# Kernel tuning notes

Hardware: AMD Instinct MI355X
Metric: run time of the kernel (lower is better)

## Reference

```python
import jax, jax.numpy as jnp
import numpy as np

NUM_MASHUP = 50000
NUM_API = 50000
NUM_DOMAIN = 500
MC = 768   # mashup_embed_channels
AC = 768   # api_embed_channels
DC = 768   # domain_embed_channels
FEAT = 128 # feature_dim
BETA = 0.5
NLAYERS = 3
E = 1600000  # bipartite invocations (one direction)
BATCH = 1024


def setup_inputs() -> dict:
    key = jax.random.key(0)
    ks = jax.random.split(key, 16)
    s = 0.02
    return {
        "x": jax.random.normal(ks[0], (BATCH, MC), dtype=jnp.float32),
        "mashup_embed": jax.random.normal(ks[1], (NUM_MASHUP, MC), dtype=jnp.float32),
        "domain_embed": jax.random.normal(ks[2], (NUM_DOMAIN, DC), dtype=jnp.float32),
        "api_embed": jax.random.normal(ks[3], (NUM_API, AC), dtype=jnp.float32),
        "W_sde": jax.random.normal(ks[4], (MC, FEAT), dtype=jnp.float32) * s,
        "b_sde": jnp.zeros((FEAT,), jnp.float32),
        "W_val": jax.random.normal(ks[5], (DC, FEAT), dtype=jnp.float32) * s,
        "b_val": jnp.zeros((FEAT,), jnp.float32),
        "W_key": jax.random.normal(ks[6], (DC, FEAT), dtype=jnp.float32) * s,
        "b_key": jnp.zeros((FEAT,), jnp.float32),
        "W_sie": jax.random.normal(ks[7], (AC, FEAT), dtype=jnp.float32) * s,
        "b_sie": jnp.zeros((FEAT,), jnp.float32),
        "edge_src": jax.random.randint(ks[8], (E,), 0, NUM_MASHUP, dtype=jnp.int32),
        "edge_dst": jax.random.randint(ks[9], (E,), 0, NUM_API, dtype=jnp.int32),
    }


def _sig_lin(h, W, b):
    # nn.Linear + Sigmoid
    return jax.nn.sigmoid(h @ W + b)


def _lightgcn(emb, row, col, num_nodes, num_layers):
    # PyG LightGCN.get_embedding: mean of layer-0..L embeddings with
    # symmetric gcn_norm propagation over the bipartite graph.
    ones = jnp.ones(row.shape, emb.dtype)
    deg = jax.ops.segment_sum(ones, row, num_segments=num_nodes)
    dinv = jnp.where(deg > 0, jax.lax.rsqrt(deg), 0.0)
    norm = dinv[row] * dinv[col]  # [2E]
    alpha = 1.0 / (num_layers + 1)
    x_l = emb
    out = emb * alpha
    for _ in range(num_layers):
        # message x[row]*norm scattered to col (graph is symmetric)
        x_l = jax.ops.segment_sum(x_l[row] * norm[:, None], col, num_segments=num_nodes)
        out = out + x_l * alpha
    return out


def reference(x, mashup_embed, domain_embed, api_embed,
              W_sde, b_sde, W_val, b_val, W_key, b_key, W_sie, b_sie,
              edge_src, edge_dst):
    batch = x.shape[0]
    # --- attention pooling over domain embeddings (SDE branch) ---
    v_mi = _sig_lin(x, W_sde, b_sde)                 # [B, F]
    v_value = _sig_lin(domain_embed, W_val, b_val)   # [D, F]
    v_key = _sig_lin(domain_embed, W_key, b_key)     # [D, F]
    al = v_mi @ v_key.T                              # [B, D]
    alpha = al / jnp.sum(al, axis=1, keepdims=True)  # normalized (no softmax)
    s_m = alpha @ v_value                            # [B, F]
    z_m = (1.0 - BETA) * s_m + BETA * v_mi           # [B, F]
    # --- LightGCN propagation over mashup-api bipartite graph ---
    v_m = _sig_lin(mashup_embed, W_sde, b_sde)       # [Nm, F]
    v_s = _sig_lin(api_embed, W_sie, b_sie)          # [Na, F]
    emb = jnp.concatenate([v_m, v_s], axis=0)        # [N, F]
    num_nodes = NUM_MASHUP + NUM_API
    src = edge_src.astype(jnp.int32)
    dst = edge_dst.astype(jnp.int32) + NUM_MASHUP
    row = jnp.concatenate([src, dst])                # [2E] symmetric edges
    col = jnp.concatenate([dst, src])
    out = _lightgcn(emb, row, col, num_nodes, NLAYERS)
    O = out[NUM_MASHUP:]                             # [Na, F]
    # --- dot-product scoring ---
    pred = z_m @ O.T                                 # [B, Na]
    return pred
```

## Files before the change

### kernel.cpp

```cpp
#include <hip/hip_runtime.h>
#include <hip/hip_bf16.h>
#include <cstddef>
#include <cstdint>

#define NM 50000
#define NA 50000
#define ND 500
#define FEAT 128
#define KDIM 768
#define BATCH 1024
#define NEDGE 1600000
#define MD 128

#define NBIN 196
#define CAP 10240
#define F1B 400
#define F1E (NEDGE / F1B)

#define PB64 782

typedef __bf16 bf16_t;
typedef bf16_t bf16x8 __attribute__((ext_vector_type(8)));
typedef bf16_t bf16x4 __attribute__((ext_vector_type(4)));
typedef float f32x4 __attribute__((ext_vector_type(4)));
typedef float f32x2 __attribute__((ext_vector_type(2)));
typedef unsigned short u16;
typedef unsigned char u8;

__device__ __forceinline__ float sigf(float x) { return 1.0f / (1.0f + __expf(-x)); }

__device__ __forceinline__ float4 dec4fp8(uint32_t w) {
  f32x2 lo = __builtin_amdgcn_cvt_pk_f32_fp8(w, false);
  f32x2 hi = __builtin_amdgcn_cvt_pk_f32_fp8(w, true);
  return make_float4(lo[0], lo[1], hi[0], hi[1]);
}
__device__ __forceinline__ u8 enc1fp8(float a) {
  return (u8)(__builtin_amdgcn_cvt_pk_fp8_f32(a, a, 0, false) & 0xff);
}

__global__ __launch_bounds__(256) void fill_bin(
    const int* __restrict__ src, const int* __restrict__ dst,
    int* __restrict__ bcur, uint32_t* __restrict__ rec )
{
  __shared__ uint32_t edg[F1E];
  __shared__ int hist[2 * NBIN];
  __shared__ int base[2 * NBIN];
  const int tid = threadIdx.x;
  for (int i = tid; i < 2 * NBIN; i += 256) hist[i] = 0;
  __syncthreads();
  const int e0 = blockIdx.x * F1E;
  for (int i = tid; i < F1E; i += 256) {
    int s = __builtin_nontemporal_load(&src[e0 + i]);
    int d = __builtin_nontemporal_load(&dst[e0 + i]);
    edg[i] = ((uint32_t)s << 16) | (uint32_t)d;
    atomicAdd(&hist[s >> 8], 1);
    atomicAdd(&hist[NBIN + (d >> 8)], 1);
  }
  __syncthreads();
  for (int i = tid; i < 2 * NBIN; i += 256) {
    int c = hist[i];
    base[i] = c ? atomicAdd(&bcur[i], c) : 0;
    hist[i] = 0;
  }
  __syncthreads();
  for (int i = tid; i < F1E; i += 256) {
    uint32_t e = edg[i];
    int s = (int)(e >> 16), d = (int)(e & 0xffffu);
    int bm = s >> 8, ba = NBIN + (d >> 8);
    int rm = base[bm] + atomicAdd(&hist[bm], 1);
    int ra = base[ba] + atomicAdd(&hist[ba], 1);
    if (rm < CAP) rec[(size_t)bm * CAP + rm] = e;
    if (ra < CAP) rec[(size_t)ba * CAP + ra] = ((uint32_t)d << 16) | (uint32_t)s;
  }
}

__global__ __launch_bounds__(256) void fill_ell2(
    const uint32_t* __restrict__ rec, const int* __restrict__ bcur,
    u16* __restrict__ adjm, u16* __restrict__ adja,
    int* __restrict__ cnt_m, int* __restrict__ cnt_a)
{
  __shared__ int cnt256[256];
  const int g = blockIdx.x;
  const int side = g >= NBIN;
  const int bin = side ? g - NBIN : g;
  u16* adj = side ? adja : adjm;
  int* cnt = side ? cnt_a : cnt_m;
  cnt256[threadIdx.x] = 0;
  __syncthreads();
  int n = bcur[g]; if (n > CAP) n = CAP;
  const uint32_t* rb = rec + (size_t)g * CAP;
  for (int i = threadIdx.x; i < n; i += 256) {
    uint32_t r = rb[i];
    int node = (int)(r >> 16);
    int rk = atomicAdd(&cnt256[node & 255], 1);
    if (rk < MD) adj[(size_t)node * MD + rk] = (u16)(r & 0xffffu);
  }
  __syncthreads();
  int node = bin * 256 + threadIdx.x;
  if (node < NM) cnt[node] = cnt256[threadIdx.x];
}

__global__ __launch_bounds__(256) void util_kernel(
    const float* __restrict__ W0, const float* __restrict__ W1,
    const float* __restrict__ W2, const float* __restrict__ W3,
    bf16_t* __restrict__ T0, bf16_t* __restrict__ T1,
    bf16_t* __restrict__ T2, bf16_t* __restrict__ T3,
    const int* __restrict__ cnt_m, const int* __restrict__ cnt_a,
    float* __restrict__ dm, float* __restrict__ da)
{
  const int b = blockIdx.x;
  if (b < 512) {
    const float* W = (b < 128) ? W0 : (b < 256) ? W1 : (b < 384) ? W2 : W3;
    bf16_t* T      = (b < 128) ? T0 : (b < 256) ? T1 : (b < 384) ? T2 : T3;
    int c = b & 127;
    for (int k = threadIdx.x; k < KDIM; k += 256)
      T[(size_t)c * KDIM + k] = (bf16_t)W[(size_t)k * FEAT + c];
  } else {
    int i = (b - 512) * 256 + threadIdx.x;
    if (i < NM) { int c = cnt_m[i]; dm[i] = c > 0 ? rsqrtf((float)c) : 0.f; }
    if (i < NA) { int c = cnt_a[i]; da[i] = c > 0 ? rsqrtf((float)c) : 0.f; }
  }
}

template<int OM>
__device__ __forceinline__ void proj_body(
    const float* __restrict__ A, const bf16_t* __restrict__ Wt,
    const float* __restrict__ bias, void* __restrict__ Cout, int M, int rowBase,
    const float* __restrict__ rowscale, bf16_t* __restrict__ C2)
{
  __shared__ bf16x8 sm[768];
  const int tid = threadIdx.x;
  const int lane = tid & 63;
  const int wid = tid >> 6;

  f32x4 acc[2][4];
  #pragma unroll
  for (int m = 0; m < 2; ++m)
    #pragma unroll
    for (int n = 0; n < 4; ++n)
      acc[m][n] = (f32x4){0.f, 0.f, 0.f, 0.f};

  const int arow = ((tid >> 6) << 4) + (tid & 15);
  const int k8 = (tid >> 4) & 3;
  int arg = rowBase + arow; if (arg > M - 1) arg = M - 1;
  const float*  aptr  = A  + (size_t)arg * KDIM + k8 * 8;
  const bf16_t* bptr0 = Wt + (size_t)arow * KDIM + k8 * 8;
  const bf16_t* bptr1 = Wt + (size_t)(arow + 64) * KDIM + k8 * 8;

  float4 pa0 = *(const float4*)aptr;
  float4 pa1 = *(const float4*)(aptr + 4);
  bf16x8 pb0 = *(const bf16x8*)bptr0;
  bf16x8 pb1 = *(const bf16x8*)bptr1;

  const int fm0 = (wid >> 1) * 2, fn0 = (wid & 1) * 4;

  for (int kt = 0; kt < KDIM / 32; ++kt) {
    bf16x8 w;
    w[0] = (bf16_t)pa0.x; w[1] = (bf16_t)pa0.y; w[2] = (bf16_t)pa0.z; w[3] = (bf16_t)pa0.w;
    w[4] = (bf16_t)pa1.x; w[5] = (bf16_t)pa1.y; w[6] = (bf16_t)pa1.z; w[7] = (bf16_t)pa1.w;
    sm[tid] = w;
    sm[256 + tid] = pb0;
    sm[512 + tid] = pb1;
    __syncthreads();
    if (kt + 1 < KDIM / 32) {
      const int ko = (kt + 1) * 32;
      pa0 = *(const float4*)(aptr + ko);
      pa1 = *(const float4*)(aptr + ko + 4);
      pb0 = *(const bf16x8*)(bptr0 + ko);
      pb1 = *(const bf16x8*)(bptr1 + ko);
    }
    bf16x8 a[2], b[4];
    #pragma unroll
    for (int m = 0; m < 2; ++m) a[m] = sm[(fm0 + m) * 64 + lane];
    #pragma unroll
    for (int n = 0; n < 4; ++n) b[n] = sm[256 + (fn0 + n) * 64 + lane];
    #pragma unroll
    for (int m = 0; m < 2; ++m)
      #pragma unroll
      for (int n = 0; n < 4; ++n)
        acc[m][n] = __builtin_amdgcn_mfma_f32_16x16x32_bf16(a[m], b[n], acc[m][n], 0, 0, 0);
    __syncthreads();
  }

  const int wRow = (wid >> 1) * 32, wCol = (wid & 1) * 64;
  const int r0 = (lane >> 4) * 4, cc = lane & 15;
  #pragma unroll
  for (int n = 0; n < 4; ++n) {
    int col = wCol + n * 16 + cc;
    float bb = bias[col];
    #pragma unroll
    for (int m = 0; m < 2; ++m) {
      #pragma unroll
      for (int r = 0; r < 4; ++r) {
        int row = rowBase + wRow + m * 16 + r0 + r;
        if (row < M) {
          float v = sigf(acc[m][n][r] + bb);
          float sc = rowscale ? rowscale[row] : 1.0f;
          if constexpr (OM == 2)
            ((u8*)Cout)[(size_t)row * FEAT + col] = enc1fp8(v * sc);
          else
            ((float*)Cout)[(size_t)row * FEAT + col] = v * sc;
          if (C2) C2[(size_t)row * FEAT + col] = (bf16_t)(0.25f * v);
        }
      }
    }
  }
}

__global__ __launch_bounds__(256) void proj_all(
    const float* __restrict__ mashup, const float* __restrict__ api,
    const float* __restrict__ x, const float* __restrict__ domain,
    const bf16_t* __restrict__ wt0, const bf16_t* __restrict__ wt1,
    const bf16_t* __restrict__ wt2, const bf16_t* __restrict__ wt3,
    const float* __restrict__ bsde, const float* __restrict__ bkey,
    const float* __restrict__ bval, const float* __restrict__ bsie,
    u8* __restrict__ M0y8, u8* __restrict__ y0a8,
    float* __restrict__ vmi, float* __restrict__ vkey, float* __restrict__ vval,
    const float* __restrict__ dm, const float* __restrict__ da,
    bf16_t* __restrict__ outA)
{
  const int b = blockIdx.x;
  if (b < PB64)
    proj_body<2>(mashup, wt0, bsde, M0y8, NM, b * 64, dm, nullptr);
  else if (b < 2 * PB64)
    proj_body<2>(api, wt3, bsie, y0a8, NA, (b - PB64) * 64, da, outA);
  else if (b < 2 * PB64 + 16)
    proj_body<0>(x, wt0, bsde, vmi, BATCH, (b - 2 * PB64) * 64, nullptr, nullptr);
  else if (b < 2 * PB64 + 24)
    proj_body<0>(domain, wt1, bkey, vkey, ND, (b - 2 * PB64 - 16) * 64, nullptr, nullptr);
  else
    proj_body<0>(domain, wt2, bval, vval, ND, (b - 2 * PB64 - 24) * 64, nullptr, nullptr);
}

__global__ __launch_bounds__(256) void attn_kernel(
    const float* __restrict__ vmi, const float* __restrict__ vkey,
    const float* __restrict__ vval, bf16_t* __restrict__ zm)
{
  const int i = blockIdx.x;
  const int tid = threadIdx.x;
  __shared__ float vs[FEAT];
  __shared__ float al[ND];
  __shared__ float red[4];
  __shared__ float ps[256];
  __shared__ float totS;
  if (tid < FEAT) vs[tid] = vmi[(size_t)i * FEAT + tid];
  __syncthreads();
  float part = 0.f;
  for (int j = tid; j < ND; j += 256) {
    const float* kr = vkey + (size_t)j * FEAT;
    float dot = 0.f;
    #pragma unroll 8
    for (int k = 0; k < FEAT; k += 4) {
      float4 kv = *(const float4*)(kr + k);
      dot += vs[k] * kv.x + vs[k + 1] * kv.y + vs[k + 2] * kv.z + vs[k + 3] * kv.w;
    }
    al[j] = dot;
    part += dot;
  }
  #pragma unroll
  for (int o = 32; o > 0; o >>= 1) part += __shfl_down(part, o, 64);
  if ((tid & 63) == 0) red[tid >> 6] = part;
  __syncthreads();
  if (tid == 0) totS = red[0] + red[1] + red[2] + red[3];
  const int f = tid & 127, h = tid >> 7;
  float s = 0.f;
  const float* vv = vval + (size_t)h * 250 * FEAT + f;
  #pragma unroll 5
  for (int j = 0; j < 250; ++j) s += al[h * 250 + j] * vv[(size_t)j * FEAT];
  ps[tid] = s;
  __syncthreads();
  if (tid < FEAT) {
    float z = 0.5f * ((ps[tid] + ps[128 + tid]) / totS + vs[tid]);
    zm[(size_t)i * FEAT + tid] = (bf16_t)z;
  }
}

__device__ __forceinline__ float4 gatherF8(const uint32_t* __restrict__ base32,
                                           const u16* __restrict__ row,
                                           int n, int half)
{
  float4 acc = make_float4(0.f, 0.f, 0.f, 0.f);
  int j = half;
  while (j + 14 < n) {
    int u[8];
    #pragma unroll
    for (int q = 0; q < 8; ++q) u[q] = row[j + 2 * q];
    uint32_t w[8];
    #pragma unroll
    for (int q = 0; q < 8; ++q) w[q] = base32[(size_t)u[q] * 32];
    #pragma unroll
    for (int q = 0; q < 8; ++q) {
      float4 v = dec4fp8(w[q]);
      acc.x += v.x; acc.y += v.y; acc.z += v.z; acc.w += v.w;
    }
    j += 16;
  }
  while (j < n) {
    float4 v = dec4fp8(base32[(size_t)row[j] * 32]);
    acc.x += v.x; acc.y += v.y; acc.z += v.z; acc.w += v.w;
    j += 2;
  }
  return acc;
}

#define REDUCE_HALVES(acc)                    \
  acc.x += __shfl_xor(acc.x, 32);             \
  acc.y += __shfl_xor(acc.y, 32);             \
  acc.z += __shfl_xor(acc.z, 32);             \
  acc.w += __shfl_xor(acc.w, 32);

__global__ __launch_bounds__(256) void prop_p1(
    const uint32_t* __restrict__ M0y8, const uint32_t* __restrict__ y0a8,
    uint32_t* __restrict__ y01a8,
    const u16* __restrict__ adja, const int* __restrict__ cnt_a,
    const float* __restrict__ da)
{
  const int a = blockIdx.x * 4 + (threadIdx.x >> 6);
  const int lane = threadIdx.x & 63;
  const int half = lane >> 5, sl = lane & 31;
  int n = cnt_a[a]; if (n > MD) n = MD;
  float4 acc = gatherF8(M0y8 + sl, adja + (size_t)a * MD, n, half);
  REDUCE_HALVES(acc)
  if (half == 0) {
    const float d = da[a];
    const float s2 = d * d;
    float4 b = dec4fp8(y0a8[(size_t)a * 32 + sl]);
    uint32_t o = __builtin_amdgcn_cvt_pk_fp8_f32(b.x + s2 * acc.x, b.y + s2 * acc.y, 0, false);
    o = __builtin_amdgcn_cvt_pk_fp8_f32(b.z + s2 * acc.z, b.w + s2 * acc.w, o, true);
    y01a8[(size_t)a * 32 + sl] = o;
  }
}

__global__ __launch_bounds__(256) void prop_p2(
    const uint32_t* __restrict__ y01a8, const uint32_t* __restrict__ M0y8,
    uint32_t* __restrict__ Sy8,
    const u16* __restrict__ adjm, const int* __restrict__ cnt_m,
    const float* __restrict__ dm)
{
  const int m = blockIdx.x * 4 + (threadIdx.x >> 6);
  const int lane = threadIdx.x & 63;
  const int half = lane >> 5, sl = lane & 31;
  int n = cnt_m[m]; if (n > MD) n = MD;
  float4 acc = gatherF8(y01a8 + sl, adjm + (size_t)m * MD, n, half);
  REDUCE_HALVES(acc)
  if (half == 0) {
    const float d = dm[m];
    const float s2 = d * d;
    float4 b = dec4fp8(M0y8[(size_t)m * 32 + sl]);
    uint32_t o = __builtin_amdgcn_cvt_pk_fp8_f32(b.x + s2 * acc.x, b.y + s2 * acc.y, 0, false);
    o = __builtin_amdgcn_cvt_pk_fp8_f32(b.z + s2 * acc.z, b.w + s2 * acc.w, o, true);
    Sy8[(size_t)m * 32 + sl] = o;
  }
}

__global__ __launch_bounds__(256) void prop_p3(
    const uint32_t* __restrict__ Sy8, const bf16_t* __restrict__ outA,
    bf16_t* __restrict__ Obf,
    const u16* __restrict__ adja, const int* __restrict__ cnt_a,
    const float* __restrict__ da)
{
  const int a = blockIdx.x * 4 + (threadIdx.x >> 6);
  const int lane = threadIdx.x & 63;
  const int half = lane >> 5, sl = lane & 31;
  int n = cnt_a[a]; if (n > MD) n = MD;
  float4 acc = gatherF8(Sy8 + sl, adja + (size_t)a * MD, n, half);
  REDUCE_HALVES(acc)
  if (half == 0) {
    const float q = 0.25f * da[a];
    bf16x4 pv = *(const bf16x4*)(outA + (size_t)a * FEAT + 4 * sl);
    bf16x4 o;
    o[0] = (bf16_t)((float)pv[0] + q * acc.x);
    o[1] = (bf16_t)((float)pv[1] + q * acc.y);
    o[2] = (bf16_t)((float)pv[2] + q * acc.z);
    o[3] = (bf16_t)((float)pv[3] + q * acc.w);
    *(bf16x4*)(Obf + (size_t)a * FEAT + 4 * sl) = o;
  }
}

__global__ __launch_bounds__(256) void pred_mfma(
    const bf16_t* __restrict__ Z, const bf16_t* __restrict__ O,
    float* __restrict__ out)
{
  const int lane = threadIdx.x & 63;
  const int wid = threadIdx.x >> 6;
  const int nBase = blockIdx.x * 256 + wid * 64;
  const int cc = lane & 15;
  const int kOff = (lane >> 4) * 8;

  bf16x8 b[4][4];
  #pragma unroll
  for (int n = 0; n < 4; ++n) {
    int c = nBase + n * 16 + cc;
    if (c > NA - 1) c = NA - 1;
    #pragma unroll
    for (int kk = 0; kk < 4; ++kk)
      b[n][kk] = *(const bf16x8*)(O + (size_t)c * FEAT + kk * 32 + kOff);
  }

  const int r0 = (lane >> 4) * 4;
  #pragma unroll
  for (int it = 0; it < 4; ++it) {
    const int iBase = blockIdx.y * 256 + it * 64;
    f32x4 acc[4][4];
    #pragma unroll
    for (int m = 0; m < 4; ++m)
      #pragma unroll
      for (int n = 0; n < 4; ++n)
        acc[m][n] = (f32x4){0.f, 0.f, 0.f, 0.f};

    #pragma unroll
    for (int kk = 0; kk < 4; ++kk) {
      bf16x8 a[4];
      #pragma unroll
      for (int m = 0; m < 4; ++m)
        a[m] = *(const bf16x8*)(Z + (size_t)(iBase + cc + m * 16) * FEAT + kk * 32 + kOff);
      #pragma unroll
      for (int m = 0; m < 4; ++m)
        #pragma unroll
        for (int n = 0; n < 4; ++n)
          acc[m][n] = __builtin_amdgcn_mfma_f32_16x16x32_bf16(a[m], b[n][kk], acc[m][n], 0, 0, 0);
    }

    #pragma unroll
    for (int n = 0; n < 4; ++n) {
      int col = nBase + n * 16 + cc;
      if (col < NA) {
        #pragma unroll
        for (int m = 0; m < 4; ++m) {
          #pragma unroll
          for (int r = 0; r < 4; ++r) {
            int row = iBase + m * 16 + r0 + r;
            __builtin_nontemporal_store(acc[m][n][r], &out[(size_t)row * NA + col]);
          }
        }
      }
    }
  }
}

static inline char* alignup(char* p, size_t a) {
  return (char*)(((uintptr_t)p + a - 1) & ~(uintptr_t)(a - 1));
}

extern "C" void kernel_launch(void* const* d_in, const int* in_sizes, int n_in,
                              void* d_out, int out_size, void* d_ws, size_t ws_size,
                              hipStream_t stream) {
  const float* x      = (const float*)d_in[0];
  const float* mashup = (const float*)d_in[1];
  const float* domain = (const float*)d_in[2];
  const float* api    = (const float*)d_in[3];
  const float* Wsde   = (const float*)d_in[4];
  const float* bsde   = (const float*)d_in[5];
  const float* Wval   = (const float*)d_in[6];
  const float* bval   = (const float*)d_in[7];
  const float* Wkey   = (const float*)d_in[8];
  const float* bkey   = (const float*)d_in[9];
  const float* Wsie   = (const float*)d_in[10];
  const float* bsie   = (const float*)d_in[11];
  const int* esrc     = (const int*)d_in[12];
  const int* edst     = (const int*)d_in[13];
  float* out = (float*)d_out;

  char* p = (char*)d_ws;
  u8*     M0y8  = (u8*)p; p += (size_t)NM * FEAT;
  u8*     y0a8  = (u8*)p; p += (size_t)NA * FEAT;
  u8*     y01a8 = (u8*)p; p += (size_t)NA * FEAT;
  u8*     Sy8   = (u8*)p; p += (size_t)NM * FEAT;
  bf16_t* outA  = (bf16_t*)p; p += (size_t)NA * FEAT * 2;
  bf16_t* Obf   = (bf16_t*)p; p += (size_t)NA * FEAT * 2;
  u16*    adjm  = (u16*)p;    p += (size_t)NM * MD * 2;
  u16*    adja  = (u16*)p;    p += (size_t)NA * MD * 2;
  float*  vmi   = (float*)p;  p += (size_t)BATCH * FEAT * 4;
  float*  vkey  = (float*)p;  p += (size_t)ND * FEAT * 4;
  float*  vval  = (float*)p;  p += (size_t)ND * FEAT * 4;
  bf16_t* zm    = (bf16_t*)p; p += (size_t)BATCH * FEAT * 2;
  int* cnt_m = (int*)p; p += (size_t)NM * 4;
  int* cnt_a = (int*)p; p += (size_t)NA * 4;
  float* dm  = (float*)p; p += (size_t)NM * 4;
  float* da  = (float*)p; p += (size_t)NA * 4;
  int* bcur  = (int*)p; p += 512 * 4;
  p = alignup(p, 16);
  bf16_t* wt0 = (bf16_t*)p; p += (size_t)FEAT * KDIM * 2;
  bf16_t* wt1 = (bf16_t*)p; p += (size_t)FEAT * KDIM * 2;
  bf16_t* wt2 = (bf16_t*)p; p += (size_t)FEAT * KDIM * 2;
  bf16_t* wt3 = (bf16_t*)p; p += (size_t)FEAT * KDIM * 2;
  uint32_t* rec = (uint32_t*)M0y8;

  hipMemsetAsync(bcur, 0, 512 * sizeof(int), stream);

  fill_bin<<<F1B, 256, 0, stream>>>(esrc, edst, bcur, rec);
  fill_ell2<<<2 * NBIN, 256, 0, stream>>>(rec, bcur, adjm, adja, cnt_m, cnt_a);
  util_kernel<<<512 + (NM + 255) / 256, 256, 0, stream>>>(
      Wsde, Wkey, Wval, Wsie, wt0, wt1, wt2, wt3, cnt_m, cnt_a, dm, da);

  proj_all<<<2 * PB64 + 32, 256, 0, stream>>>(
      mashup, api, x, domain, wt0, wt1, wt2, wt3,
      bsde, bkey, bval, bsie, M0y8, y0a8, vmi, vkey, vval, dm, da, outA);

  attn_kernel<<<BATCH, 256, 0, stream>>>(vmi, vkey, vval, zm);

  prop_p1<<<NA / 4, 256, 0, stream>>>((const uint32_t*)M0y8, (const uint32_t*)y0a8,
                                      (uint32_t*)y01a8, adja, cnt_a, da);
  prop_p2<<<NM / 4, 256, 0, stream>>>((const uint32_t*)y01a8, (const uint32_t*)M0y8,
                                      (uint32_t*)Sy8, adjm, cnt_m, dm);
  prop_p3<<<NA / 4, 256, 0, stream>>>((const uint32_t*)Sy8, outA, Obf,
                                      adja, cnt_a, da);

  pred_mfma<<<dim3((NA + 255) / 256, BATCH / 256), 256, 0, stream>>>(zm, Obf, out);
}
```

Before: 421.3 us.

## Rewrite projection GEMM as per-wave 16-row tiles without shared memory

The projection kernel no longer stages A and W tiles through LDS with block-wide barriers. Each wave now computes a 16x128 output tile on its own, loading A rows directly into registers and reading the transposed bf16 weights straight from global memory (L2/L1 cached) for all 8 column fragments. This removes the __syncthreads and LDS traffic. In exchange, each wave issues more global weight loads, since W is no longer shared across the 4 waves of a block, and it holds more accumulator registers.

```diff
diff --git a/kernel.cpp b/kernel.cpp
--- a/kernel.cpp
+++ b/kernel.cpp
@@ -123,85 +123,60 @@
 }
 
 template<int OM>
-__device__ __forceinline__ void proj_body(
+__device__ __forceinline__ void proj_wave(
     const float* __restrict__ A, const bf16_t* __restrict__ Wt,
     const float* __restrict__ bias, void* __restrict__ Cout, int M, int rowBase,
     const float* __restrict__ rowscale, bf16_t* __restrict__ C2)
 {
-  __shared__ bf16x8 sm[768];
-  const int tid = threadIdx.x;
-  const int lane = tid & 63;
-  const int wid = tid >> 6;
-
-  f32x4 acc[2][4];
+  const int lane = threadIdx.x & 63;
+  const int r = lane & 15;
+  const int kg = (lane >> 4) * 8;
+
+  int rowL = rowBase + r; if (rowL > M - 1) rowL = M - 1;
+  const float*  ap = A  + (size_t)rowL * KDIM + kg;
+  const bf16_t* bp = Wt + (size_t)r * KDIM + kg;
+
+  f32x4 acc[8];
   #pragma unroll
-  for (int m = 0; m < 2; ++m)
-    #pragma unroll
-    for (int n = 0; n < 4; ++n)
-      acc[m][n] = (f32x4){0.f, 0.f, 0.f, 0.f};
-
-  const int arow = ((tid >> 6) << 4) + (tid & 15);
-  const int k8 = (tid >> 4) & 3;
-  int arg = rowBase + arow; if (arg > M - 1) arg = M - 1;
-  const float*  aptr  = A  + (size_t)arg * KDIM + k8 * 8;
-  const bf16_t* bptr0 = Wt + (size_t)arow * KDIM + k8 * 8;
-  const bf16_t* bptr1 = Wt + (size_t)(arow + 64) * KDIM + k8 * 8;
-
-  float4 pa0 = *(const float4*)aptr;
-  float4 pa1 = *(const float4*)(aptr + 4);
-  bf16x8 pb0 = *(const bf16x8*)bptr0;
-  bf16x8 pb1 = *(const bf16x8*)bptr1;
-
-  const int fm0 = (wid >> 1) * 2, fn0 = (wid & 1) * 4;
+  for (int n = 0; n < 8; ++n) acc[n] = (f32x4){0.f, 0.f, 0.f, 0.f};
+
+  float4 pa0 = *(const float4*)ap;
+  float4 pa1 = *(const float4*)(ap + 4);
 
   for (int kt = 0; kt < KDIM / 32; ++kt) {
-    bf16x8 w;
-    w[0] = (bf16_t)pa0.x; w[1] = (bf16_t)pa0.y; w[2] = (bf16_t)pa0.z; w[3] = (bf16_t)pa0.w;
-    w[4] = (bf16_t)pa1.x; w[5] = (bf16_t)pa1.y; w[6] = (bf16_t)pa1.z; w[7] = (bf16_t)pa1.w;
-    sm[tid] = w;
-    sm[256 + tid] = pb0;
-    sm[512 + tid] = pb1;
-    __syncthreads();
+    const int k0 = kt * 32;
+    bf16x8 a;
+    a[0] = (bf16_t)pa0.x; a[1] = (bf16_t)pa0.y; a[2] = (bf16_t)pa0.z; a[3] = (bf16_t)pa0.w;
+    a[4] = (bf16_t)pa1.x; a[5] = (bf16_t)pa1.y; a[6] = (bf16_t)pa1.z; a[7] = (bf16_t)pa1.w;
     if (kt + 1 < KDIM / 32) {
-      const int ko = (kt + 1) * 32;
-      pa0 = *(const float4*)(aptr + ko);
-      pa1 = *(const float4*)(aptr + ko + 4);
-      pb0 = *(const bf16x8*)(bptr0 + ko);
-      pb1 = *(const bf16x8*)(bptr1 + ko);
-    }
-    bf16x8 a[2], b[4];
-    #pragma unroll
-    for (int m = 0; m < 2; ++m) a[m] = sm[(fm0 + m) * 64 + lane];
-    #pragma unroll
-    for (int n = 0; n < 4; ++n) b[n] = sm[256 + (fn0 + n) * 64 + lane];
-    #pragma unroll
-    for (int m = 0; m < 2; ++m)
-      #pragma unroll
-      for (int n = 0; n < 4; ++n)
-        acc[m][n] = __builtin_amdgcn_mfma_f32_16x16x32_bf16(a[m], b[n], acc[m][n], 0, 0, 0);
-    __syncthreads();
-  }
-
-  const int wRow = (wid >> 1) * 32, wCol = (wid & 1) * 64;
-  const int r0 = (lane >> 4) * 4, cc = lane & 15;
+      pa0 = *(const float4*)(ap + k0 + 32);
+      pa1 = *(const float4*)(ap + k0 + 36);
+    }
+    bf16x8 b[8];
+    #pragma unroll
+    for (int n = 0; n < 8; ++n)
+      b[n] = *(const bf16x8*)(bp + (size_t)n * 16 * KDIM + k0);
+    #pragma unroll
+    for (int n = 0; n < 8; ++n)
+      acc[n] = __builtin_amdgcn_mfma_f32_16x16x32_bf16(a, b[n], acc[n], 0, 0, 0);
+  }
+
+  const int r0 = (lane >> 4) * 4;
   #pragma unroll
-  for (int n = 0; n < 4; ++n) {
-    int col = wCol + n * 16 + cc;
+  for (int n = 0; n < 8; ++n) {
+    int col = n * 16 + r;
     float bb = bias[col];
     #pragma unroll
-    for (int m = 0; m < 2; ++m) {
-      #pragma unroll
-      for (int r = 0; r < 4; ++r) {
-        int row = rowBase + wRow + m * 16 + r0 + r;
-        if (row < M) {
-          float v = sigf(acc[m][n][r] + bb);
-          float sc = rowscale ? rowscale[row] : 1.0f;
-          if constexpr (OM == 2)
-            ((u8*)Cout)[(size_t)row * FEAT + col] = enc1fp8(v * sc);
-          else
-            ((float*)Cout)[(size_t)row * FEAT + col] = v * sc;
-          if (C2) C2[(size_t)row * FEAT + col] = (bf16_t)(0.25f * v);
-        }
+    for (int rr = 0; rr < 4; ++rr) {
+      int row = rowBase + r0 + rr;
+      if (row < M) {
+        float v = sigf(acc[n][rr] + bb);
+        float sc = rowscale ? rowscale[row] : 1.0f;
+        if constexpr (OM == 2)
+          ((u8*)Cout)[(size_t)row * FEAT + col] = enc1fp8(v * sc);
+        else
+          ((float*)Cout)[(size_t)row * FEAT + col] = v * sc;
+        if (C2) C2[(size_t)row * FEAT + col] = (bf16_t)(0.25f * v);
       }
     }
   }
@@ -220,16 +195,17 @@
     bf16_t* __restrict__ outA)
 {
   const int b = blockIdx.x;
+  const int w = threadIdx.x >> 6;
   if (b < PB64)
-    proj_body<2>(mashup, wt0, bsde, M0y8, NM, b * 64, dm, nullptr);
+    proj_wave<2>(mashup, wt0, bsde, M0y8, NM, b * 64 + w * 16, dm, nullptr);
   else if (b < 2 * PB64)
-    proj_body<2>(api, wt3, bsie, y0a8, NA, (b - PB64) * 64, da, outA);
+    proj_wave<2>(api, wt3, bsie, y0a8, NA, (b - PB64) * 64 + w * 16, da, outA);
   else if (b < 2 * PB64 + 16)
-    proj_body<0>(x, wt0, bsde, vmi, BATCH, (b - 2 * PB64) * 64, nullptr, nullptr);
+    proj_wave<0>(x, wt0, bsde, vmi, BATCH, (b - 2 * PB64) * 64 + w * 16, nullptr, nullptr);
   else if (b < 2 * PB64 + 24)
-    proj_body<0>(domain, wt1, bkey, vkey, ND, (b - 2 * PB64 - 16) * 64, nullptr, nullptr);
+    proj_wave<0>(domain, wt1, bkey, vkey, ND, (b - 2 * PB64 - 16) * 64 + w * 16, nullptr, nullptr);
   else
-    proj_body<0>(domain, wt2, bval, vval, ND, (b - 2 * PB64 - 24) * 64, nullptr, nullptr);
+    proj_wave<0>(domain, wt2, bval, vval, ND, (b - 2 * PB64 - 24) * 64 + w * 16, nullptr, nullptr);
 }
 
 __global__ __launch_bounds__(256) void attn_kernel(
```

Measured after the change: 534.2 us. 26.8% more time.

## Double-buffer projection GEMM tiles with direct global-to-LDS loads

Applied to the files above, without the earlier changes.

The projection GEMM now loads A (fp32) and W tiles straight into LDS with global_load_lds, double-buffered, and waits on vmcnt so the next tile's load overlaps the current tile's MFMAs. The fp32-to-bf16 conversion of A moves from the store side to the LDS read side. This removes the register staging round trip and one sync per iteration, but doubles LDS use and relies on hand-written waitcnt and barrier ordering being correct.

```diff
diff --git a/kernel.cpp b/kernel.cpp
--- a/kernel.cpp
+++ b/kernel.cpp
@@ -18,6 +18,7 @@
 #define F1E (NEDGE / F1B)
 
 #define PB64 782
+#define PKT  24
 
 typedef __bf16 bf16_t;
 typedef bf16_t bf16x8 __attribute__((ext_vector_type(8)));
@@ -36,6 +37,12 @@
 }
 __device__ __forceinline__ u8 enc1fp8(float a) {
   return (u8)(__builtin_amdgcn_cvt_pk_fp8_f32(a, a, 0, false) & 0xff);
+}
+
+__device__ __forceinline__ void gll16(const void* g, void* l) {
+  __builtin_amdgcn_global_load_lds(
+      (const __attribute__((address_space(1))) unsigned int*)g,
+      (__attribute__((address_space(3))) unsigned int*)l, 16, 0, 0);
 }
 
 __global__ __launch_bounds__(256) void fill_bin(
@@ -128,11 +135,16 @@
     const float* __restrict__ bias, void* __restrict__ Cout, int M, int rowBase,
     const float* __restrict__ rowscale, bf16_t* __restrict__ C2)
 {
-  __shared__ bf16x8 sm[768];
+  __shared__ alignas(16) char smraw[2][16384];
   const int tid = threadIdx.x;
   const int lane = tid & 63;
   const int wid = tid >> 6;
 
+  int arow = rowBase + wid * 16 + (lane & 15); if (arow > M - 1) arow = M - 1;
+  const float*  asrc  = A  + (size_t)arow * KDIM + ((lane >> 4) * 8);
+  const bf16_t* bsrc0 = Wt + (size_t)((2 * wid) * 16 + (lane & 15)) * KDIM + ((lane >> 4) * 8);
+  const bf16_t* bsrc1 = Wt + (size_t)((2 * wid + 1) * 16 + (lane & 15)) * KDIM + ((lane >> 4) * 8);
+
   f32x4 acc[2][4];
   #pragma unroll
   for (int m = 0; m < 2; ++m)
@@ -140,46 +152,56 @@
     for (int n = 0; n < 4; ++n)
       acc[m][n] = (f32x4){0.f, 0.f, 0.f, 0.f};
 
-  const int arow = ((tid >> 6) << 4) + (tid & 15);
-  const int k8 = (tid >> 4) & 3;
-  int arg = rowBase + arow; if (arg > M - 1) arg = M - 1;
-  const float*  aptr  = A  + (size_t)arg * KDIM + k8 * 8;
-  const bf16_t* bptr0 = Wt + (size_t)arow * KDIM + k8 * 8;
-  const bf16_t* bptr1 = Wt + (size_t)(arow + 64) * KDIM + k8 * 8;
-
-  float4 pa0 = *(const float4*)aptr;
-  float4 pa1 = *(const float4*)(aptr + 4);
-  bf16x8 pb0 = *(const bf16x8*)bptr0;
-  bf16x8 pb1 = *(const bf16x8*)bptr1;
-
-  const int fm0 = (wid >> 1) * 2, fn0 = (wid & 1) * 4;
-
-  for (int kt = 0; kt < KDIM / 32; ++kt) {
-    bf16x8 w;
-    w[0] = (bf16_t)pa0.x; w[1] = (bf16_t)pa0.y; w[2] = (bf16_t)pa0.z; w[3] = (bf16_t)pa0.w;
-    w[4] = (bf16_t)pa1.x; w[5] = (bf16_t)pa1.y; w[6] = (bf16_t)pa1.z; w[7] = (bf16_t)pa1.w;
-    sm[tid] = w;
-    sm[256 + tid] = pb0;
-    sm[512 + tid] = pb1;
-    __syncthreads();
-    if (kt + 1 < KDIM / 32) {
-      const int ko = (kt + 1) * 32;
-      pa0 = *(const float4*)(aptr + ko);
-      pa1 = *(const float4*)(aptr + ko + 4);
-      pb0 = *(const bf16x8*)(bptr0 + ko);
-      pb1 = *(const bf16x8*)(bptr1 + ko);
-    }
+  const int fA = (wid >> 1) * 2;
+  const int fB = (wid & 1) * 4;
+
+  int cur = 0;
+  {
+    char* base = smraw[0];
+    gll16(asrc,      base + wid * 2048);
+    gll16(asrc + 4,  base + wid * 2048 + 1024);
+    gll16(bsrc0,     base + 8192 + (2 * wid) * 1024);
+    gll16(bsrc1,     base + 8192 + (2 * wid + 1) * 1024);
+  }
+
+  for (int kt = 0; kt < PKT; ++kt) {
+    if (kt + 1 < PKT) {
+      const int k0 = (kt + 1) * 32;
+      char* base = smraw[cur ^ 1];
+      gll16(asrc + k0,      base + wid * 2048);
+      gll16(asrc + k0 + 4,  base + wid * 2048 + 1024);
+      gll16(bsrc0 + k0,     base + 8192 + (2 * wid) * 1024);
+      gll16(bsrc1 + k0,     base + 8192 + (2 * wid + 1) * 1024);
+      asm volatile("s_waitcnt vmcnt(4)" ::: "memory");
+    } else {
+      asm volatile("s_waitcnt vmcnt(0)" ::: "memory");
+    }
+    __builtin_amdgcn_s_barrier();
+    asm volatile("" ::: "memory");
+
+    const char* bb = smraw[cur];
     bf16x8 a[2], b[4];
     #pragma unroll
-    for (int m = 0; m < 2; ++m) a[m] = sm[(fm0 + m) * 64 + lane];
-    #pragma unroll
-    for (int n = 0; n < 4; ++n) b[n] = sm[256 + (fn0 + n) * 64 + lane];
+    for (int m = 0; m < 2; ++m) {
+      f32x4 lo = *(const f32x4*)(bb + (fA + m) * 2048 + lane * 16);
+      f32x4 hi = *(const f32x4*)(bb + (fA + m) * 2048 + 1024 + lane * 16);
+      bf16x8 t;
+      t[0] = (bf16_t)lo[0]; t[1] = (bf16_t)lo[1]; t[2] = (bf16_t)lo[2]; t[3] = (bf16_t)lo[3];
+      t[4] = (bf16_t)hi[0]; t[5] = (bf16_t)hi[1]; t[6] = (bf16_t)hi[2]; t[7] = (bf16_t)hi[3];
+      a[m] = t;
+    }
+    #pragma unroll
+    for (int n = 0; n < 4; ++n)
+      b[n] = *(const bf16x8*)(bb + 8192 + (fB + n) * 1024 + lane * 16);
     #pragma unroll
     for (int m = 0; m < 2; ++m)
       #pragma unroll
       for (int n = 0; n < 4; ++n)
         acc[m][n] = __builtin_amdgcn_mfma_f32_16x16x32_bf16(a[m], b[n], acc[m][n], 0, 0, 0);
-    __syncthreads();
+
+    asm volatile("" ::: "memory");
+    __builtin_amdgcn_s_barrier();
+    cur ^= 1;
   }
 
   const int wRow = (wid >> 1) * 32, wCol = (wid & 1) * 64;
```

Result: slower. 454.2 us (+7.8%).
